# Performance work log

Measured on AMD Instinct MI355X. Metric: run time of the kernel, lower is better.

## Reference

```python
import math
import jax, jax.numpy as jnp
import numpy as np

N_HEADS = 16

def setup_inputs() -> dict:
    key = jax.random.key(0)
    qkv = jax.random.normal(key, (4, 3072, 2048), dtype=jnp.float32)
    return {"qkv": qkv}

def reference(qkv):
    bs, width, length = qkv.shape
    ch = width // (3 * N_HEADS)
    # [bs*H, 3*ch, L] -> split into q, k, v of [bs*H, ch, L]
    qkv_r = qkv.reshape(bs * N_HEADS, 3 * ch, length)
    q, k, v = qkv_r[:, :ch], qkv_r[:, ch:2 * ch], qkv_r[:, 2 * ch:]
    scale = 1.0 / math.sqrt(math.sqrt(ch))
    # scores: [bs*H, T, S]
    weight = jnp.einsum('bct,bcs->bts', q * scale, k * scale)
    weight = jax.nn.softmax(weight, axis=-1)
    a = jnp.einsum('bts,bcs->bct', weight, v)
    return a.reshape(bs, -1, length)
```

## Files before the change

### kernel.cpp

```cpp
#include <hip/hip_runtime.h>
#include <cstdint>

typedef _Float16 half8 __attribute__((ext_vector_type(8)));
typedef __fp16 fp16x2 __attribute__((ext_vector_type(2)));
typedef float f32x4 __attribute__((ext_vector_type(4)));

#define HSTRIDE 131072
#define KOFF    ((size_t)64 * HSTRIDE)
#define VOFF    ((size_t)128 * HSTRIDE)

__device__ __forceinline__ float fast_exp2(float x) {
    return __builtin_amdgcn_exp2f(x);
}

__device__ __forceinline__ uint32_t pkrtz(float a, float b) {
    fp16x2 h = __builtin_amdgcn_cvt_pkrtz(a, b);
    return __builtin_bit_cast(uint32_t, h);
}

__device__ __forceinline__ void load_lds16(const _Float16* g, _Float16* l) {
    auto* g1 = reinterpret_cast<const __attribute__((address_space(1))) uint32_t*>(
        reinterpret_cast<uintptr_t>(g));
    auto* l3 = reinterpret_cast<__attribute__((address_space(3))) uint32_t*>(
        reinterpret_cast<uintptr_t>(l));
    __builtin_amdgcn_global_load_lds(g1, l3, 16, 0, 0);
}

__global__ __launch_bounds__(256) void prep_kernel(const float* __restrict__ qkv,
                                                   _Float16* __restrict__ ws)
{
    __shared__ float Lf[64 * 67];

    const int tid  = threadIdx.x;
    const int lane = tid & 63;
    const int wave = tid >> 6;
    const int bid  = blockIdx.x;

    if (bid < 2048) {
        const int head  = (bid >> 5) & 63;
        const int chunk = bid & 31;
        const int b4 = head >> 4, h = head & 15;
        const float* src = qkv + (((size_t)(b4 * 3072 + h * 192 + 64)) << 11)
                         + chunk * 64;

#pragma unroll
        for (int k = 0; k < 4; ++k) {
            int idx = k * 256 + tid;
            int c = idx >> 4;
            int t4 = (idx & 15) << 2;
            float4 f = *(const float4*)&src[(((size_t)c) << 11) + t4];
            float* d = &Lf[c * 67 + t4];
            d[0] = f.x; d[1] = f.y; d[2] = f.z; d[3] = f.w;
        }
        __syncthreads();

        const int q = lane >> 4, l15 = lane & 15;
        const int scol = wave * 16 + l15;
#pragma unroll
        for (int k = 0; k < 2; ++k) {
            uint32_t d[4];
#pragma unroll
            for (int j = 0; j < 4; ++j) {
                float a = Lf[(32 * k + 8 * q + 2 * j) * 67 + scol];
                float b = Lf[(32 * k + 8 * q + 2 * j + 1) * 67 + scol];
                d[j] = pkrtz(a, b);
            }
            size_t off = KOFF + (size_t)head * HSTRIDE
                       + (size_t)((((chunk * 4 + wave) * 2 + k) * 512) + lane * 8);
            *(uint4*)&ws[off] = make_uint4(d[0], d[1], d[2], d[3]);
        }
    } else {
        const int vb = bid - 2048;
        const int head = vb >> 5, chunk = vb & 31;
        const int b4 = head >> 4, h = head & 15;
        const float* src = qkv + (((size_t)(b4 * 3072 + h * 192 + 128)) << 11) + chunk * 64;
        const int q = lane >> 4, cl = lane & 15;
        const int c = wave * 16 + cl;
#pragma unroll
        for (int k = 0; k < 2; ++k) {
            const float* p = &src[((size_t)c << 11) + k * 32 + q * 4];
            float4 f0 = *(const float4*)&p[0];
            float4 f1 = *(const float4*)&p[16];
            size_t off = VOFF + (size_t)head * HSTRIDE
                       + (size_t)(((chunk * 2 + k) * 4 + wave) * 512 + lane * 8);
            *(uint4*)&ws[off] = make_uint4(pkrtz(f0.x, f0.y), pkrtz(f0.z, f0.w),
                                           pkrtz(f1.x, f1.y), pkrtz(f1.x * 0.f + f1.z, f1.w));
        }
    }
}

__launch_bounds__(256, 2)
__global__ void attn_kernel(const float* __restrict__ qkv,
                            const _Float16* __restrict__ ws, float* __restrict__ out)
{
    __shared__ __align__(16) _Float16 sK[3][4096];
    __shared__ __align__(16) _Float16 sV[3][4096];

    const int tid  = threadIdx.x;
    const int lane = tid & 63;
    const int wave = tid >> 6;
    const int l15  = lane & 15;
    const int quad = lane >> 4;

    const int bid  = blockIdx.x;
    const int head = bid & 63;
    const int tblk = bid >> 6;
    const int T0   = tblk * 256;
    const int b4   = head >> 4;
    const int h    = head & 15;

    const _Float16* Kt = ws + KOFF + (size_t)head * HSTRIDE;
    const _Float16* Vt = ws + VOFF + (size_t)head * HSTRIDE;
    const float*    Qg = qkv + ((size_t)(b4 * 3072 + h * 192) << 11);
    const float kQ = 0.125f * 1.44269504088896340736f;

    f32x4 Oacc[4][4];
#pragma unroll
    for (int ct = 0; ct < 4; ++ct)
#pragma unroll
        for (int nt = 0; nt < 4; ++nt) Oacc[ct][nt] = (f32x4)0.f;
    f32x4 Lacc[4];
#pragma unroll
    for (int nt = 0; nt < 4; ++nt) Lacc[nt] = (f32x4)0.f;
    const f32x4 fz = (f32x4)0.f;

    half8 ones;
#pragma unroll
    for (int j = 0; j < 8; ++j) ones[j] = (_Float16)1.0f;

    const int lb = lane * 8;

    auto stage = [&](int buf, int tile) {
        const _Float16* kg = Kt + (size_t)tile * 4096 + wave * 1024 + lane * 8;
        const _Float16* vg = Vt + (size_t)tile * 4096 + wave * 1024 + lane * 8;
        load_lds16(kg,       &sK[buf][wave * 1024]);
        load_lds16(kg + 512, &sK[buf][wave * 1024 + 512]);
        load_lds16(vg,       &sV[buf][wave * 1024]);
        load_lds16(vg + 512, &sV[buf][wave * 1024 + 512]);
    };

    stage(0, 0);
    stage(1, 1);

    half8 qb[4][2];
#pragma unroll
    for (int nt = 0; nt < 4; ++nt) {
        const int t = T0 + wave * 64 + nt * 16 + l15;
#pragma unroll
        for (int ks = 0; ks < 2; ++ks) {
            float f[8];
#pragma unroll
            for (int j = 0; j < 8; ++j)
                f[j] = Qg[((size_t)(ks * 32 + quad * 8 + j) << 11) + t];
            uint4 u = make_uint4(pkrtz(f[0] * kQ, f[1] * kQ), pkrtz(f[2] * kQ, f[3] * kQ),
                                 pkrtz(f[4] * kQ, f[5] * kQ), pkrtz(f[6] * kQ, f[7] * kQ));
            qb[nt][ks] = __builtin_bit_cast(half8, u);
        }
    }

    half8 pf[2][4];

    auto computeS = [&](const _Float16* sKb) {
        half8 kf[4][2];
#pragma unroll
        for (int mt = 0; mt < 4; ++mt)
#pragma unroll
            for (int ks = 0; ks < 2; ++ks)
                kf[mt][ks] = *(const half8*)&sKb[(mt * 2 + ks) * 512 + lb];
#pragma unroll
        for (int sc2 = 0; sc2 < 2; ++sc2) {
            f32x4 Sa[4], Sb[4];
#pragma unroll
            for (int nt = 0; nt < 4; ++nt) {
                f32x4 t0 = __builtin_amdgcn_mfma_f32_16x16x32_f16(kf[2 * sc2][0], qb[nt][0], fz, 0, 0, 0);
                Sa[nt]   = __builtin_amdgcn_mfma_f32_16x16x32_f16(kf[2 * sc2][1], qb[nt][1], t0, 0, 0, 0);
                f32x4 t1 = __builtin_amdgcn_mfma_f32_16x16x32_f16(kf[2 * sc2 + 1][0], qb[nt][0], fz, 0, 0, 0);
                Sb[nt]   = __builtin_amdgcn_mfma_f32_16x16x32_f16(kf[2 * sc2 + 1][1], qb[nt][1], t1, 0, 0, 0);
            }
#pragma unroll
            for (int nt = 0; nt < 4; ++nt) {
                float e0 = fast_exp2(Sa[nt][0]);
                float e1 = fast_exp2(Sa[nt][1]);
                float e2 = fast_exp2(Sa[nt][2]);
                float e3 = fast_exp2(Sa[nt][3]);
                float e4 = fast_exp2(Sb[nt][0]);
                float e5 = fast_exp2(Sb[nt][1]);
                float e6 = fast_exp2(Sb[nt][2]);
                float e7 = fast_exp2(Sb[nt][3]);
                uint4 u = make_uint4(pkrtz(e0, e1), pkrtz(e2, e3),
                                     pkrtz(e4, e5), pkrtz(e6, e7));
                pf[sc2][nt] = __builtin_bit_cast(half8, u);
            }
        }
    };

    auto computeO = [&](const _Float16* sVb) {
        half8 vf[2][4];
#pragma unroll
        for (int sc2 = 0; sc2 < 2; ++sc2)
#pragma unroll
            for (int ct = 0; ct < 4; ++ct)
                vf[sc2][ct] = *(const half8*)&sVb[(sc2 * 4 + ct) * 512 + lb];
#pragma unroll
        for (int ct = 0; ct < 4; ++ct)
#pragma unroll
            for (int sc2 = 0; sc2 < 2; ++sc2)
#pragma unroll
                for (int nt = 0; nt < 4; ++nt)
                    Oacc[ct][nt] = __builtin_amdgcn_mfma_f32_16x16x32_f16(
                        vf[sc2][ct], pf[sc2][nt], Oacc[ct][nt], 0, 0, 0);
#pragma unroll
        for (int sc2 = 0; sc2 < 2; ++sc2)
#pragma unroll
            for (int nt = 0; nt < 4; ++nt)
                Lacc[nt] = __builtin_amdgcn_mfma_f32_16x16x32_f16(
                    ones, pf[sc2][nt], Lacc[nt], 0, 0, 0);
    };

    __builtin_amdgcn_s_waitcnt(0);
    __syncthreads();
    computeS(sK[0]);

    int bV = 0;
    for (int it = 0; it < 31; ++it) {
        __builtin_amdgcn_s_waitcnt(0);
        __syncthreads();
        if (it < 30) {
            int bs_ = bV + 2; if (bs_ >= 3) bs_ -= 3;
            stage(bs_, it + 2);
        }
        int bK = bV + 1; if (bK >= 3) bK -= 3;
        computeO(sV[bV]);
        computeS(sK[bK]);
        bV = bK;
    }

    computeO(sV[bV]);

    float inv[4];
#pragma unroll
    for (int nt = 0; nt < 4; ++nt) inv[nt] = 1.f / Lacc[nt][0];

    float* ob = out + (((size_t)(b4 * 1024 + h * 64)) << 11) + T0 + wave * 64;
#pragma unroll
    for (int ct = 0; ct < 4; ++ct)
#pragma unroll
        for (int nt = 0; nt < 4; ++nt) {
            f32x4 o = Oacc[ct][nt];
#pragma unroll
            for (int r = 0; r < 4; ++r)
                ob[((size_t)(ct * 16 + quad * 4 + r) << 11) + nt * 16 + l15] = o[r] * inv[nt];
        }
}

extern "C" void kernel_launch(void* const* d_in, const int* in_sizes, int n_in,
                              void* d_out, int out_size, void* d_ws, size_t ws_size,
                              hipStream_t stream) {
    const float* qkv = (const float*)d_in[0];
    float* out = (float*)d_out;
    _Float16* ws = (_Float16*)d_ws;
    prep_kernel<<<dim3(4096), dim3(256), 0, stream>>>(qkv, ws);
    attn_kernel<<<dim3(512), dim3(256), 0, stream>>>(qkv, ws, out);
}
```

Before: 213.5 us.

## Software-pipeline QK^T MFMAs with exp2 interleaved into PV accumulation

Restructures the main loop so each iteration issues all S=K^T·Q MFMAs for the next tile first. It then interleaves the PV/rowsum MFMAs for the previous tile with the exp2/pack of the new scores, per column tile. Ping-pong P-fragment buffers (pfA/pfB) with a two-way unrolled loop avoid register copies. The aim is to overlap transcendental VALU work with matrix-core work. In exchange it keeps more S accumulators live, which raises register pressure at 2 waves/SIMD. It also removes a dummy multiply in the V conversion.

```diff
diff --git a/kernel.cpp b/kernel.cpp
--- a/kernel.cpp
+++ b/kernel.cpp
@@ -84,7 +84,7 @@
             size_t off = VOFF + (size_t)head * HSTRIDE
                        + (size_t)(((chunk * 2 + k) * 4 + wave) * 512 + lane * 8);
             *(uint4*)&ws[off] = make_uint4(pkrtz(f0.x, f0.y), pkrtz(f0.z, f0.w),
-                                           pkrtz(f1.x, f1.y), pkrtz(f1.x * 0.f + f1.z, f1.w));
+                                           pkrtz(f1.x, f1.y), pkrtz(f1.z, f1.w));
         }
     }
 }
@@ -158,71 +158,10 @@
         }
     }
 
-    half8 pf[2][4];
-
-    auto computeS = [&](const _Float16* sKb) {
-        half8 kf[4][2];
-#pragma unroll
-        for (int mt = 0; mt < 4; ++mt)
-#pragma unroll
-            for (int ks = 0; ks < 2; ++ks)
-                kf[mt][ks] = *(const half8*)&sKb[(mt * 2 + ks) * 512 + lb];
-#pragma unroll
-        for (int sc2 = 0; sc2 < 2; ++sc2) {
-            f32x4 Sa[4], Sb[4];
-#pragma unroll
-            for (int nt = 0; nt < 4; ++nt) {
-                f32x4 t0 = __builtin_amdgcn_mfma_f32_16x16x32_f16(kf[2 * sc2][0], qb[nt][0], fz, 0, 0, 0);
-                Sa[nt]   = __builtin_amdgcn_mfma_f32_16x16x32_f16(kf[2 * sc2][1], qb[nt][1], t0, 0, 0, 0);
-                f32x4 t1 = __builtin_amdgcn_mfma_f32_16x16x32_f16(kf[2 * sc2 + 1][0], qb[nt][0], fz, 0, 0, 0);
-                Sb[nt]   = __builtin_amdgcn_mfma_f32_16x16x32_f16(kf[2 * sc2 + 1][1], qb[nt][1], t1, 0, 0, 0);
-            }
-#pragma unroll
-            for (int nt = 0; nt < 4; ++nt) {
-                float e0 = fast_exp2(Sa[nt][0]);
-                float e1 = fast_exp2(Sa[nt][1]);
-                float e2 = fast_exp2(Sa[nt][2]);
-                float e3 = fast_exp2(Sa[nt][3]);
-                float e4 = fast_exp2(Sb[nt][0]);
-                float e5 = fast_exp2(Sb[nt][1]);
-                float e6 = fast_exp2(Sb[nt][2]);
-                float e7 = fast_exp2(Sb[nt][3]);
-                uint4 u = make_uint4(pkrtz(e0, e1), pkrtz(e2, e3),
-                                     pkrtz(e4, e5), pkrtz(e6, e7));
-                pf[sc2][nt] = __builtin_bit_cast(half8, u);
-            }
-        }
-    };
-
-    auto computeO = [&](const _Float16* sVb) {
-        half8 vf[2][4];
-#pragma unroll
-        for (int sc2 = 0; sc2 < 2; ++sc2)
-#pragma unroll
-            for (int ct = 0; ct < 4; ++ct)
-                vf[sc2][ct] = *(const half8*)&sVb[(sc2 * 4 + ct) * 512 + lb];
-#pragma unroll
-        for (int ct = 0; ct < 4; ++ct)
-#pragma unroll
-            for (int sc2 = 0; sc2 < 2; ++sc2)
-#pragma unroll
-                for (int nt = 0; nt < 4; ++nt)
-                    Oacc[ct][nt] = __builtin_amdgcn_mfma_f32_16x16x32_f16(
-                        vf[sc2][ct], pf[sc2][nt], Oacc[ct][nt], 0, 0, 0);
-#pragma unroll
-        for (int sc2 = 0; sc2 < 2; ++sc2)
-#pragma unroll
-            for (int nt = 0; nt < 4; ++nt)
-                Lacc[nt] = __builtin_amdgcn_mfma_f32_16x16x32_f16(
-                    ones, pf[sc2][nt], Lacc[nt], 0, 0, 0);
-    };
-
-    __builtin_amdgcn_s_waitcnt(0);
-    __syncthreads();
-    computeS(sK[0]);
-
+    half8 pfA[2][4], pfB[2][4];
     int bV = 0;
-    for (int it = 0; it < 31; ++it) {
+
+    auto body = [&](int it, half8 (&PFo)[2][4], half8 (&PFn)[2][4]) {
         __builtin_amdgcn_s_waitcnt(0);
         __syncthreads();
         if (it < 30) {
@@ -230,12 +169,119 @@
             stage(bs_, it + 2);
         }
         int bK = bV + 1; if (bK >= 3) bK -= 3;
-        computeO(sV[bV]);
-        computeS(sK[bK]);
+        const _Float16* sKb = sK[bK];
+        const _Float16* sVb = sV[bV];
+
+        half8 kf[4][2];
+#pragma unroll
+        for (int mt = 0; mt < 4; ++mt)
+#pragma unroll
+            for (int ks = 0; ks < 2; ++ks)
+                kf[mt][ks] = *(const half8*)&sKb[(mt * 2 + ks) * 512 + lb];
+
+        f32x4 Sa[2][4], Sb[2][4];
+#pragma unroll
+        for (int sc2 = 0; sc2 < 2; ++sc2)
+#pragma unroll
+            for (int nt = 0; nt < 4; ++nt) {
+                f32x4 t0 = __builtin_amdgcn_mfma_f32_16x16x32_f16(kf[2 * sc2][0], qb[nt][0], fz, 0, 0, 0);
+                Sa[sc2][nt] = __builtin_amdgcn_mfma_f32_16x16x32_f16(kf[2 * sc2][1], qb[nt][1], t0, 0, 0, 0);
+                f32x4 t1 = __builtin_amdgcn_mfma_f32_16x16x32_f16(kf[2 * sc2 + 1][0], qb[nt][0], fz, 0, 0, 0);
+                Sb[sc2][nt] = __builtin_amdgcn_mfma_f32_16x16x32_f16(kf[2 * sc2 + 1][1], qb[nt][1], t1, 0, 0, 0);
+            }
+
+#pragma unroll
+        for (int ct = 0; ct < 4; ++ct) {
+            half8 vf0 = *(const half8*)&sVb[(0 * 4 + ct) * 512 + lb];
+            half8 vf1 = *(const half8*)&sVb[(1 * 4 + ct) * 512 + lb];
+#pragma unroll
+            for (int nt = 0; nt < 4; ++nt) {
+                Oacc[ct][nt] = __builtin_amdgcn_mfma_f32_16x16x32_f16(
+                    vf0, PFo[0][nt], Oacc[ct][nt], 0, 0, 0);
+                Oacc[ct][nt] = __builtin_amdgcn_mfma_f32_16x16x32_f16(
+                    vf1, PFo[1][nt], Oacc[ct][nt], 0, 0, 0);
+            }
+            Lacc[ct] = __builtin_amdgcn_mfma_f32_16x16x32_f16(ones, PFo[0][ct], Lacc[ct], 0, 0, 0);
+            Lacc[ct] = __builtin_amdgcn_mfma_f32_16x16x32_f16(ones, PFo[1][ct], Lacc[ct], 0, 0, 0);
+
+            {
+                float e0 = fast_exp2(Sa[0][ct][0]);
+                float e1 = fast_exp2(Sa[0][ct][1]);
+                float e2 = fast_exp2(Sa[0][ct][2]);
+                float e3 = fast_exp2(Sa[0][ct][3]);
+                float e4 = fast_exp2(Sb[0][ct][0]);
+                float e5 = fast_exp2(Sb[0][ct][1]);
+                float e6 = fast_exp2(Sb[0][ct][2]);
+                float e7 = fast_exp2(Sb[0][ct][3]);
+                uint4 u = make_uint4(pkrtz(e0, e1), pkrtz(e2, e3),
+                                     pkrtz(e4, e5), pkrtz(e6, e7));
+                PFn[0][ct] = __builtin_bit_cast(half8, u);
+            }
+            {
+                float e0 = fast_exp2(Sa[1][ct][0]);
+                float e1 = fast_exp2(Sa[1][ct][1]);
+                float e2 = fast_exp2(Sa[1][ct][2]);
+                float e3 = fast_exp2(Sa[1][ct][3]);
+                float e4 = fast_exp2(Sb[1][ct][0]);
+                float e5 = fast_exp2(Sb[1][ct][1]);
+                float e6 = fast_exp2(Sb[1][ct][2]);
+                float e7 = fast_exp2(Sb[1][ct][3]);
+                uint4 u = make_uint4(pkrtz(e0, e1), pkrtz(e2, e3),
+                                     pkrtz(e4, e5), pkrtz(e6, e7));
+                PFn[1][ct] = __builtin_bit_cast(half8, u);
+            }
+        }
         bV = bK;
-    }
-
-    computeO(sV[bV]);
+    };
+
+    __builtin_amdgcn_s_waitcnt(0);
+    __syncthreads();
+    {
+        half8 kf[4][2];
+#pragma unroll
+        for (int mt = 0; mt < 4; ++mt)
+#pragma unroll
+            for (int ks = 0; ks < 2; ++ks)
+                kf[mt][ks] = *(const half8*)&sK[0][(mt * 2 + ks) * 512 + lb];
+#pragma unroll
+        for (int sc2 = 0; sc2 < 2; ++sc2)
+#pragma unroll
+            for (int nt = 0; nt < 4; ++nt) {
+                f32x4 t0 = __builtin_amdgcn_mfma_f32_16x16x32_f16(kf[2 * sc2][0], qb[nt][0], fz, 0, 0, 0);
+                f32x4 Sa = __builtin_amdgcn_mfma_f32_16x16x32_f16(kf[2 * sc2][1], qb[nt][1], t0, 0, 0, 0);
+                f32x4 t1 = __builtin_amdgcn_mfma_f32_16x16x32_f16(kf[2 * sc2 + 1][0], qb[nt][0], fz, 0, 0, 0);
+                f32x4 Sb = __builtin_amdgcn_mfma_f32_16x16x32_f16(kf[2 * sc2 + 1][1], qb[nt][1], t1, 0, 0, 0);
+                uint4 u = make_uint4(pkrtz(fast_exp2(Sa[0]), fast_exp2(Sa[1])),
+                                     pkrtz(fast_exp2(Sa[2]), fast_exp2(Sa[3])),
+                                     pkrtz(fast_exp2(Sb[0]), fast_exp2(Sb[1])),
+                                     pkrtz(fast_exp2(Sb[2]), fast_exp2(Sb[3])));
+                pfA[sc2][nt] = __builtin_bit_cast(half8, u);
+            }
+    }
+
+    for (int it = 0; it < 30; it += 2) {
+        body(it,     pfA, pfB);
+        body(it + 1, pfB, pfA);
+    }
+    body(30, pfA, pfB);
+
+    {
+        const _Float16* sVb = sV[bV];
+#pragma unroll
+        for (int ct = 0; ct < 4; ++ct) {
+            half8 vf0 = *(const half8*)&sVb[(0 * 4 + ct) * 512 + lb];
+            half8 vf1 = *(const half8*)&sVb[(1 * 4 + ct) * 512 + lb];
+#pragma unroll
+            for (int nt = 0; nt < 4; ++nt) {
+                Oacc[ct][nt] = __builtin_amdgcn_mfma_f32_16x16x32_f16(
+                    vf0, pfB[0][nt], Oacc[ct][nt], 0, 0, 0);
+                Oacc[ct][nt] = __builtin_amdgcn_mfma_f32_16x16x32_f16(
+                    vf1, pfB[1][nt], Oacc[ct][nt], 0, 0, 0);
+            }
+            Lacc[ct] = __builtin_amdgcn_mfma_f32_16x16x32_f16(ones, pfB[0][ct], Lacc[ct], 0, 0, 0);
+            Lacc[ct] = __builtin_amdgcn_mfma_f32_16x16x32_f16(ones, pfB[1][ct], Lacc[ct], 0, 0, 0);
+        }
+    }
 
     float inv[4];
 #pragma unroll
```

Result: no change. 215.9 us (+1.1%).
